# Kernel tuning notes

Hardware: AMD Instinct MI355X
Metric: run time of the kernel (lower is better)

Reference implementation:

```python
import jax, jax.numpy as jnp
import numpy as np

ANNEAL_T_START = 5.0
T_END = 1.0


def setup_inputs() -> dict:
    key = jax.random.key(0)
    ks = jax.random.split(key, 8)
    B, V, H, CD, WID = 8192, 1024, 128, 16, 64
    return {
        "cond": jax.random.normal(ks[0], (B, CD), jnp.float32),
        "W": 0.01 * jax.random.normal(ks[1], (V, H), jnp.float32),
        "b": 0.01 * jax.random.normal(ks[2], (V,), jnp.float32),
        "c": 0.01 * jax.random.normal(ks[3], (H,), jnp.float32),
        "fc1_w": jax.random.normal(ks[4], (WID, CD), jnp.float32) / np.float32(np.sqrt(CD)),
        "fc1_b": jnp.zeros((WID,), jnp.float32),
        "fc2_w": jax.random.normal(ks[5], (2 * (V + H), WID), jnp.float32) / np.float32(np.sqrt(WID)),
        "fc2_b": jnp.zeros((2 * (V + H),), jnp.float32),
        "falloff": jnp.float32(1.0),
        "steps": 16,
    }


def _bern(key, p):
    # Bernoulli sample as float of same dtype as p.
    return (jax.random.uniform(key, p.shape, p.dtype) < p).astype(p.dtype)


def reference(cond, W, b, c, fc1_w, fc1_b, fc2_w, fc2_b, falloff, steps):
    V, H = W.shape
    B = cond.shape[0]
    dtype = W.dtype

    # Conditioner: FiLM-style modulation of visible/hidden biases.
    x = jnp.tanh(cond @ fc1_w.T + fc1_b)
    x = x @ fc2_w.T + fc2_b  # [B, 2*(V+H)]
    gamma_b = x[:, :V]
    beta_b = x[:, V:2 * V]
    gamma_c = x[:, 2 * V:2 * V + H]
    beta_c = x[:, 2 * V + H:]
    b_mod = (1.0 + gamma_b) * b + beta_b  # [B, V]
    c_mod = (1.0 + gamma_c) * c + beta_c  # [B, H]
    bsum = jnp.sum(b_mod, axis=-1)  # [B], constant across steps

    # Annealing temperature schedule (sigmoid falloff).
    t = jnp.arange(steps, dtype=dtype)
    s = 1.0 / (1.0 + jnp.exp(falloff * (t - steps / 2.0)))
    temps = T_END + (ANNEAL_T_START - T_END) * s  # [steps]

    base = jax.random.key(42)
    v0 = _bern(jax.random.fold_in(base, 2 ** 20), jnp.full((B, V), 0.5, dtype))
    s0_0 = jnp.ones((B, 1), dtype)

    def flip(v, s0):
        return s0 * v + (1.0 - s0) * (1.0 - v)

    def step(carry, xs):
        v, s0 = carry
        i, T = xs
        k1, k2, k3 = jax.random.split(jax.random.fold_in(base, i), 3)
        v_eff = flip(v, s0)
        p_h = jax.nn.sigmoid((v_eff @ W + c_mod) / T)  # [B, H]
        h = _bern(k1, p_h)
        a = h @ W.T  # [B, V]
        vb = jnp.sum(v * b_mod, axis=-1)
        va = jnp.sum(v * a, axis=-1)
        dE = -bsum - jnp.sum(a, axis=-1) + 2.0 * vb + 2.0 * va  # [B]
        p_s0 = jax.nn.sigmoid(dE / T)
        s0n = _bern(k2, p_s0)[:, None]  # [B, 1]
        p_v = jax.nn.sigmoid((a + b_mod) / T)
        v_samp = _bern(k3, p_v)
        v_next = flip(v_samp, s0n)
        return (v_next, s0n), None

    (v, _), _ = jax.lax.scan(
        step, (v0, s0_0), (jnp.arange(steps, dtype=jnp.int32), temps)
    )
    return v
```

## Files before the change

### kernel.cpp

```cpp
#include <hip/hip_runtime.h>
#include <stdint.h>

#pragma clang fp contract(off)

#define B_ 8192
#define V_ 1024
#define H_ 128
#define CD_ 16
#define WID_ 64
#define NOUT_ 2304
#define STEPS_ 16

typedef float f32x2 __attribute__((ext_vector_type(2)));

__device__ __forceinline__ void pkfma(f32x2& acc, f32x2 wv, f32x2 bf2) {
  asm("v_pk_fma_f32 %0, %1, %2, %0" : "+v"(acc) : "v"(wv), "v"(bf2));
}

__host__ __device__ __forceinline__ void tf2x32(uint32_t k0, uint32_t k1,
                                                uint32_t x0, uint32_t x1,
                                                uint32_t* o0, uint32_t* o1) {
  uint32_t ks2 = k0 ^ k1 ^ 0x1BD11BDAu;
#define RL_(v, d) (((v) << (d)) | ((v) >> (32 - (d))))
#define RND_(a) { x0 += x1; x1 = RL_(x1, a); x1 ^= x0; }
  x0 += k0; x1 += k1;
  RND_(13) RND_(15) RND_(26) RND_(6)
  x0 += k1; x1 += ks2 + 1u;
  RND_(17) RND_(29) RND_(16) RND_(24)
  x0 += ks2; x1 += k0 + 2u;
  RND_(13) RND_(15) RND_(26) RND_(6)
  x0 += k0; x1 += k1 + 3u;
  RND_(17) RND_(29) RND_(16) RND_(24)
  x0 += k1; x1 += ks2 + 4u;
  RND_(13) RND_(15) RND_(26) RND_(6)
  x0 += ks2; x1 += k0 + 5u;
#undef RND_
#undef RL_
  *o0 = x0; *o1 = x1;
}

struct Keys { uint32_t a[6]; };

__device__ __forceinline__ uint32_t draw_bits(uint32_t ka, uint32_t kb, uint32_t j) {
  uint32_t x0, x1;
  tf2x32(ka, kb, 0u, j, &x0, &x1);
  return x0 ^ x1;
}

__device__ __forceinline__ float bits_to_u(uint32_t bits) {
  return __fsub_rn(__uint_as_float((bits >> 9) | 0x3f800000u), 1.0f);
}

__device__ __forceinline__ float exp_a(float x) {
  float xc = fminf(fmaxf(x, -88.3762626647949f), 88.3762626647950f);
  float fx = floorf(__fadd_rn(__fmul_rn(xc, 1.44269504088896341f), 0.5f));
  float xr = __fsub_rn(xc, __fmul_rn(0.693359375f, fx));
  xr = __fsub_rn(xr, __fmul_rn(-2.12194440e-4f, fx));
  float zz = __fmul_rn(xr, xr);
  float y = 1.9875691500E-4f;
  y = __fadd_rn(__fmul_rn(y, xr), 1.3981999507E-3f);
  y = __fadd_rn(__fmul_rn(y, xr), 8.3334519073E-3f);
  y = __fadd_rn(__fmul_rn(y, xr), 4.1665795894E-2f);
  y = __fadd_rn(__fmul_rn(y, xr), 1.6666665459E-1f);
  y = __fadd_rn(__fmul_rn(y, xr), 5.0000001201E-1f);
  y = __fadd_rn(__fmul_rn(y, zz), xr);
  y = __fadd_rn(y, 1.0f);
  int n = (int)fx;
  float sc = __int_as_float((n + 127) << 23);
  return __fmul_rn(y, sc);
}

__device__ __forceinline__ float tanh_a(float xin) {
  float x = fmaxf(fminf(xin, 7.90531110763549805f), -7.90531110763549805f);
  float x2 = __fmul_rn(x, x);
  float p = __fadd_rn(__fmul_rn(x2, -2.76076847742355e-16f), 2.00018790482477e-13f);
  p = __fadd_rn(__fmul_rn(x2, p), -8.60467152213735e-11f);
  p = __fadd_rn(__fmul_rn(x2, p), 5.12229709037114e-08f);
  p = __fadd_rn(__fmul_rn(x2, p), 1.48572235717979e-05f);
  p = __fadd_rn(__fmul_rn(x2, p), 6.37261928875436e-04f);
  p = __fadd_rn(__fmul_rn(x2, p), 4.89352455891786e-03f);
  p = __fmul_rn(x, p);
  float q = __fadd_rn(__fmul_rn(x2, 1.19825839466702e-06f), 1.18534705686654e-04f);
  q = __fadd_rn(__fmul_rn(x2, q), 2.26843463243900e-03f);
  q = __fadd_rn(__fmul_rn(x2, q), 4.89352518554385e-03f);
  float r = p / q;
  if (fabsf(xin) < 0.0004f) r = xin;
  return r;
}

__device__ __forceinline__ float sigmoid_a(float z) {
  float e = exp_a(-z);
  return 1.0f / __fadd_rn(1.0f, e);
}

__global__ void k_transpose(const float* __restrict__ W, float* __restrict__ WT,
                            const float* __restrict__ fc2w, float* __restrict__ fc2T) {
  int i = blockIdx.x * blockDim.x + threadIdx.x;
  if (i < V_ * H_) { int v = i / H_, h = i % H_; WT[h * V_ + v] = W[i]; }
  if (i < NOUT_ * WID_) { int j = i / WID_, w = i % WID_; fc2T[w * NOUT_ + j] = fc2w[i]; }
}

__global__ void k_temps(const float* __restrict__ falloff, float* __restrict__ temps) {
  int t = threadIdx.x;
  if (t < 16) {
    float arg = __fmul_rn(*falloff, __fsub_rn((float)t, 8.0f));
    float e = exp_a(arg);
    float s = 1.0f / __fadd_rn(1.0f, e);
    temps[t] = __fadd_rn(1.0f, __fmul_rn(4.0f, s));
  }
}

__global__ void k_mlp1(const float* __restrict__ cond, const float* __restrict__ fc1w,
                       const float* __restrict__ fc1b, float* __restrict__ xout) {
  int idx = blockIdx.x * blockDim.x + threadIdx.x;
  if (idx >= B_ * WID_) return;
  int row = idx >> 6, w = idx & 63;
  float acc = 0.0f;
  for (int k = 0; k < CD_; k++) acc = __fmaf_rn(cond[row * CD_ + k], fc1w[w * CD_ + k], acc);
  float z = __fadd_rn(acc, fc1b[w]);
  xout[idx] = tanh_a(z);
}

__global__ __launch_bounds__(128) void k_mlp2b(const float* __restrict__ xmlp,
                       const float* __restrict__ fc2T, const float* __restrict__ fc2b,
                       const float* __restrict__ bvec, float* __restrict__ b_mod) {
  __shared__ float xs[32][WID_];
  int jbase = blockIdx.x * 128;
  int r0 = blockIdx.y * 32;
  int tid = threadIdx.x;
  for (int t = tid; t < 32 * WID_; t += 128)
    xs[t >> 6][t & 63] = xmlp[(r0 + (t >> 6)) * WID_ + (t & 63)];
  __syncthreads();
  int j = jbase + tid;
  float accg[32], accb[32];
#pragma unroll
  for (int r = 0; r < 32; r++) { accg[r] = 0.0f; accb[r] = 0.0f; }
  for (int w = 0; w < WID_; w++) {
    float fg = fc2T[w * NOUT_ + j];
    float fb = fc2T[w * NOUT_ + 1024 + j];
#pragma unroll
    for (int r = 0; r < 32; r++) {
      float xv = xs[r][w];
      accg[r] = __fmaf_rn(xv, fg, accg[r]);
      accb[r] = __fmaf_rn(xv, fb, accb[r]);
    }
  }
  float bj = bvec[j];
  float biasg = fc2b[j], biasb = fc2b[1024 + j];
#pragma unroll
  for (int r = 0; r < 32; r++) {
    float g = __fadd_rn(accg[r], biasg);
    float bb = __fadd_rn(accb[r], biasb);
    float t1 = __fadd_rn(1.0f, g);
    b_mod[(r0 + r) * V_ + j] = __fadd_rn(__fmul_rn(t1, bj), bb);
  }
}

__global__ __launch_bounds__(128) void k_mlp2c(const float* __restrict__ xmlp,
                       const float* __restrict__ fc2T, const float* __restrict__ fc2b,
                       const float* __restrict__ cvec, float* __restrict__ c_mod) {
  __shared__ float xs[32][WID_];
  int r0 = blockIdx.y * 32;
  int tid = threadIdx.x;
  for (int t = tid; t < 32 * WID_; t += 128)
    xs[t >> 6][t & 63] = xmlp[(r0 + (t >> 6)) * WID_ + (t & 63)];
  __syncthreads();
  float accg[32], accb[32];
#pragma unroll
  for (int r = 0; r < 32; r++) { accg[r] = 0.0f; accb[r] = 0.0f; }
  for (int w = 0; w < WID_; w++) {
    float fg = fc2T[w * NOUT_ + 2048 + tid];
    float fb = fc2T[w * NOUT_ + 2176 + tid];
#pragma unroll
    for (int r = 0; r < 32; r++) {
      float xv = xs[r][w];
      accg[r] = __fmaf_rn(xv, fg, accg[r]);
      accb[r] = __fmaf_rn(xv, fb, accb[r]);
    }
  }
  float cj = cvec[tid];
  float biasg = fc2b[2048 + tid], biasb = fc2b[2176 + tid];
#pragma unroll
  for (int r = 0; r < 32; r++) {
    float g = __fadd_rn(accg[r], biasg);
    float bb = __fadd_rn(accb[r], biasb);
    float t1 = __fadd_rn(1.0f, g);
    c_mod[(r0 + r) * H_ + tid] = __fadd_rn(__fmul_rn(t1, cj), bb);
  }
}

__global__ __launch_bounds__(64) void k_bsum(const float* __restrict__ b_mod,
                                             float* __restrict__ bsum) {
  int row = blockIdx.x * 64 + threadIdx.x;
  const float4* bp = (const float4*)(b_mod + (size_t)row * V_);
  float acc = 0.0f;
  for (int c = 0; c < 32; c++) {
    float4 Bv[8];
#pragma unroll
    for (int q = 0; q < 8; q++) Bv[q] = bp[c * 8 + q];
#pragma unroll
    for (int q = 0; q < 8; q++) {
      acc = __fadd_rn(acc, Bv[q].x);
      acc = __fadd_rn(acc, Bv[q].y);
      acc = __fadd_rn(acc, Bv[q].z);
      acc = __fadd_rn(acc, Bv[q].w);
    }
  }
  bsum[row] = acc;
}

__global__ void k_v0(float* __restrict__ vout, uint32_t* __restrict__ v_bits,
                     float* __restrict__ s0, uint32_t kva, uint32_t kvb) {
  int idx = blockIdx.x * blockDim.x + threadIdx.x;
  int row = idx >> 10, col = idx & 1023;
  uint32_t bits = draw_bits(kva, kvb, (uint32_t)idx);
  float u = bits_to_u(bits);
  float v = (u < 0.5f) ? 1.0f : 0.0f;
  vout[idx] = v;
  unsigned long long m = __ballot(v == 1.0f);
  if ((threadIdx.x & 63) == 0) {
    v_bits[row * 32 + (col >> 5)] = (uint32_t)m;
    v_bits[row * 32 + (col >> 5) + 1] = (uint32_t)(m >> 32);
  }
  if (col == 0) s0[row] = 1.0f;
}

__global__ __launch_bounds__(128) void k_h(const float* __restrict__ W,
                   const float* __restrict__ c_mod, const uint32_t* __restrict__ v_bits,
                   const float* __restrict__ s0, uint32_t* __restrict__ h_bits,
                   const float* __restrict__ temps, int step, Keys kn) {
  __shared__ uint32_t nib[16][32];
  int tid = threadIdx.x;
  int ct = tid & 31;
  int rt = tid >> 5;
  int h0 = ct << 2;
  int row0 = blockIdx.x * 16 + rt * 4;
  float T = temps[step];
  f32x2 acc[4][2];
#pragma unroll
  for (int r = 0; r < 4; r++) { acc[r][0] = f32x2{0.f, 0.f}; acc[r][1] = f32x2{0.f, 0.f}; }
  uint32_t flip[4];
#pragma unroll
  for (int r = 0; r < 4; r++) flip[r] = (s0[row0 + r] == 0.0f) ? 0xFFFFFFFFu : 0u;
  const float* wbase = W + h0;

  auto sect = [&](uint32_t w0, uint32_t w1, uint32_t w2, uint32_t w3, const float* wp) {
    uint32_t m[4];
    m[0] = __brev(w0) ^ flip[0];
    m[1] = __brev(w1) ^ flip[1];
    m[2] = __brev(w2) ^ flip[2];
    m[3] = __brev(w3) ^ flip[3];
    for (int j4 = 0; j4 < 8; j4++) {
#pragma unroll
      for (int jj = 0; jj < 4; jj++) {
        float4 wv = *(const float4*)(wp + (size_t)jj * H_);
        f32x2 wlo = {wv.x, wv.y};
        f32x2 whi = {wv.z, wv.w};
#pragma unroll
        for (int r = 0; r < 4; r++) {
          uint32_t sm = (uint32_t)((int32_t)m[r] >> 31);
          m[r] <<= 1;
          float bf = __uint_as_float(sm & 0x3f800000u);
          f32x2 b2 = {bf, bf};
          pkfma(acc[r][0], wlo, b2);
          pkfma(acc[r][1], whi, b2);
        }
      }
      wp += (size_t)4 * H_;
    }
  };

  const uint4* vb0 = (const uint4*)(v_bits + (size_t)row0 * 32);
  const uint4* vb1 = (const uint4*)(v_bits + (size_t)(row0 + 1) * 32);
  const uint4* vb2 = (const uint4*)(v_bits + (size_t)(row0 + 2) * 32);
  const uint4* vb3 = (const uint4*)(v_bits + (size_t)(row0 + 3) * 32);
  for (int kq = 0; kq < 8; kq++) {
    uint4 q0 = vb0[kq];
    uint4 q1 = vb1[kq];
    uint4 q2 = vb2[kq];
    uint4 q3 = vb3[kq];
    const float* wk = wbase + (size_t)(kq * 128) * H_;
    sect(q0.x, q1.x, q2.x, q3.x, wk);
    sect(q0.y, q1.y, q2.y, q3.y, wk + (size_t)32 * H_);
    sect(q0.z, q1.z, q2.z, q3.z, wk + (size_t)64 * H_);
    sect(q0.w, q1.w, q2.w, q3.w, wk + (size_t)96 * H_);
  }

#pragma unroll
  for (int r = 0; r < 4; r++) {
    int row = row0 + r;
    float4 cm = *(const float4*)(c_mod + (size_t)row * H_ + h0);
    const float cma[4] = {cm.x, cm.y, cm.z, cm.w};
    const float ac[4] = {acc[r][0][0], acc[r][0][1], acc[r][1][0], acc[r][1][1]};
    uint32_t nb = 0;
#pragma unroll
    for (int e = 0; e < 4; e++) {
      float z = __fadd_rn(ac[e], cma[e]) / T;
      float p = sigmoid_a(z);
      uint32_t b = draw_bits(kn.a[0], kn.a[1], (uint32_t)(row * H_ + h0 + e));
      if (bits_to_u(b) < p) nb |= 1u << e;
    }
    nib[rt * 4 + r][ct] = nb;
  }
  __syncthreads();
  if (tid < 64) {
    int rloc = tid >> 2, wq = tid & 3;
    uint32_t word = 0;
#pragma unroll
    for (int i = 0; i < 8; i++) word |= nib[rloc][wq * 8 + i] << (4 * i);
    h_bits[(size_t)(blockIdx.x * 16 + rloc) * 4 + wq] = word;
  }
}

__global__ __launch_bounds__(256) void k_a(const float* __restrict__ WT,
                   const uint32_t* __restrict__ h_bits, float* __restrict__ a) {
  int tid = threadIdx.x;
  int ct = tid & 63;
  int rt = tid >> 6;
  int v0 = blockIdx.x * 256 + (ct << 2);
  int r0 = blockIdx.y * 32 + rt * 8;
  f32x2 acc[8][2];
#pragma unroll
  for (int r = 0; r < 8; r++) { acc[r][0] = f32x2{0.f, 0.f}; acc[r][1] = f32x2{0.f, 0.f}; }
  uint4 hw[8];
#pragma unroll
  for (int r = 0; r < 8; r++) hw[r] = *(const uint4*)(h_bits + (size_t)(r0 + r) * 4);
  const float* wp0 = WT + v0;

  auto asect = [&](int WW, const uint32_t mwin[8]) {
    uint32_t m[8];
#pragma unroll
    for (int r = 0; r < 8; r++) m[r] = __brev(mwin[r]);
    const float* wp = wp0 + (size_t)(WW * 32) * V_;
    for (int j4 = 0; j4 < 8; j4++) {
#pragma unroll
      for (int jj = 0; jj < 4; jj++) {
        float4 wv = *(const float4*)(wp + (size_t)jj * V_);
        f32x2 wlo = {wv.x, wv.y};
        f32x2 whi = {wv.z, wv.w};
#pragma unroll
        for (int r = 0; r < 8; r++) {
          uint32_t sm = (uint32_t)((int32_t)m[r] >> 31);
          m[r] <<= 1;
          float bf = __uint_as_float(sm & 0x3f800000u);
          f32x2 b2 = {bf, bf};
          pkfma(acc[r][0], wlo, b2);
          pkfma(acc[r][1], whi, b2);
        }
      }
      wp += (size_t)4 * V_;
    }
  };

  {
    uint32_t mw[8];
#pragma unroll
    for (int r = 0; r < 8; r++) mw[r] = hw[r].x;
    asect(0, mw);
#pragma unroll
    for (int r = 0; r < 8; r++) mw[r] = hw[r].y;
    asect(1, mw);
#pragma unroll
    for (int r = 0; r < 8; r++) mw[r] = hw[r].z;
    asect(2, mw);
#pragma unroll
    for (int r = 0; r < 8; r++) mw[r] = hw[r].w;
    asect(3, mw);
  }

#pragma unroll
  for (int r = 0; r < 8; r++) {
    float4 o = make_float4(acc[r][0][0], acc[r][0][1], acc[r][1][0], acc[r][1][1]);
    *(float4*)(a + (size_t)(r0 + r) * V_ + v0) = o;
  }
}

__global__ __launch_bounds__(64) void k_s0(const float* __restrict__ a,
                     const float* __restrict__ b_mod, const float* __restrict__ bsum,
                     const uint32_t* __restrict__ v_bits, float* __restrict__ s0,
                     const float* __restrict__ temps, int step, Keys kn) {
  int row = blockIdx.x * 64 + threadIdx.x;
  const float4* ap = (const float4*)(a + (size_t)row * V_);
  const float4* bp = (const float4*)(b_mod + (size_t)row * V_);
  const uint32_t* vbp = v_bits + row * 32;
  float suma = 0.0f, vb = 0.0f, va = 0.0f;
  float4 A0[8], B0[8], A1[8], B1[8];
  uint32_t m0, m1;

  auto LOADC = [&](int c, float4* A, float4* B, uint32_t& m) {
#pragma unroll
    for (int q = 0; q < 8; q++) { A[q] = ap[c * 8 + q]; B[q] = bp[c * 8 + q]; }
    m = vbp[c];
  };
  auto PROC = [&](const float4* A, const float4* B, uint32_t m) {
#pragma unroll
    for (int q = 0; q < 8; q++) {
      const float ax[4] = {A[q].x, A[q].y, A[q].z, A[q].w};
      const float bx[4] = {B[q].x, B[q].y, B[q].z, B[q].w};
#pragma unroll
      for (int e = 0; e < 4; e++) {
        float bit = (float)((m >> (q * 4 + e)) & 1u);
        suma = __fadd_rn(suma, ax[e]);
        vb = __fmaf_rn(bx[e], bit, vb);
        va = __fmaf_rn(ax[e], bit, va);
      }
    }
  };

  LOADC(0, A0, B0, m0);
  for (int cc = 0; cc < 16; cc++) {
    LOADC(2 * cc + 1, A1, B1, m1);
    PROC(A0, B0, m0);
    if (cc < 15) LOADC(2 * cc + 2, A0, B0, m0);
    PROC(A1, B1, m1);
  }

  float dE = __fsub_rn(-bsum[row], suma);
  dE = __fadd_rn(dE, __fmul_rn(2.0f, vb));
  dE = __fadd_rn(dE, __fmul_rn(2.0f, va));
  float T = temps[step];
  float p = sigmoid_a(dE / T);
  uint32_t bits = draw_bits(kn.a[2], kn.a[3], (uint32_t)row);
  float u = bits_to_u(bits);
  s0[row] = (u < p) ? 1.0f : 0.0f;
}

__global__ void k_v(const float* __restrict__ a, const float* __restrict__ b_mod,
                    const float* __restrict__ s0, float* __restrict__ vout,
                    uint32_t* __restrict__ v_bits, const float* __restrict__ temps, int step,
                    Keys kn) {
  int idx = blockIdx.x * blockDim.x + threadIdx.x;
  int row = idx >> 10, col = idx & 1023;
  float T = temps[step];
  float z = __fadd_rn(a[idx], b_mod[idx]) / T;
  float p = sigmoid_a(z);
  uint32_t bits = draw_bits(kn.a[4], kn.a[5], (uint32_t)idx);
  float u = bits_to_u(bits);
  float vs = (u < p) ? 1.0f : 0.0f;
  float vn = (s0[row] != 0.0f) ? vs : (1.0f - vs);
  vout[idx] = vn;
  unsigned long long m = __ballot(vn == 1.0f);
  if ((threadIdx.x & 63) == 0) {
    v_bits[row * 32 + (col >> 5)] = (uint32_t)m;
    v_bits[row * 32 + (col >> 5) + 1] = (uint32_t)(m >> 32);
  }
}

extern "C" void kernel_launch(void* const* d_in, const int* in_sizes, int n_in,
                              void* d_out, int out_size, void* d_ws, size_t ws_size,
                              hipStream_t stream) {
  const float* cond = (const float*)d_in[0];
  const float* W = (const float*)d_in[1];
  const float* bvec = (const float*)d_in[2];
  const float* cvec = (const float*)d_in[3];
  const float* fc1w = (const float*)d_in[4];
  const float* fc1b = (const float*)d_in[5];
  const float* fc2w = (const float*)d_in[6];
  const float* fc2b = (const float*)d_in[7];
  const float* falloff = (const float*)d_in[8];
  float* out = (float*)d_out;

  char* ws = (char*)d_ws;
  size_t off = 0;
  auto alloc = [&](size_t bytes) { void* p = ws + off; off += (bytes + 255) & ~(size_t)255; return p; };
  float* b_mod = (float*)alloc((size_t)B_ * V_ * 4);
  float* c_mod = (float*)alloc((size_t)B_ * H_ * 4);
  float* abuf  = (float*)alloc((size_t)B_ * V_ * 4);
  float* xmlp  = (float*)alloc((size_t)B_ * WID_ * 4);
  float* bsum  = (float*)alloc((size_t)B_ * 4);
  float* s0    = (float*)alloc((size_t)B_ * 4);
  uint32_t* v_bits = (uint32_t*)alloc((size_t)B_ * 32 * 4);
  uint32_t* h_bits = (uint32_t*)alloc((size_t)B_ * 4 * 4);
  float* WT    = (float*)alloc((size_t)H_ * V_ * 4);
  float* fc2T  = (float*)alloc((size_t)WID_ * NOUT_ * 4);
  float* temps = (float*)alloc(16 * 4);

  uint32_t kva, kvb;
  tf2x32(0u, 42u, 0u, 1048576u, &kva, &kvb);
  Keys kn[16];
  for (int i = 0; i < 16; i++) {
    uint32_t f0, f1;
    tf2x32(0u, 42u, 0u, (uint32_t)i, &f0, &f1);
    uint32_t a0, a1;
    tf2x32(f0, f1, 0u, 0u, &a0, &a1); kn[i].a[0] = a0; kn[i].a[1] = a1;
    tf2x32(f0, f1, 0u, 1u, &a0, &a1); kn[i].a[2] = a0; kn[i].a[3] = a1;
    tf2x32(f0, f1, 0u, 2u, &a0, &a1); kn[i].a[4] = a0; kn[i].a[5] = a1;
  }

  k_transpose<<<(NOUT_ * WID_ + 255) / 256, 256, 0, stream>>>(W, WT, fc2w, fc2T);
  k_temps<<<1, 64, 0, stream>>>(falloff, temps);
  k_mlp1<<<(B_ * WID_) / 256, 256, 0, stream>>>(cond, fc1w, fc1b, xmlp);
  k_mlp2b<<<dim3(8, 256), 128, 0, stream>>>(xmlp, fc2T, fc2b, bvec, b_mod);
  k_mlp2c<<<dim3(1, 256), 128, 0, stream>>>(xmlp, fc2T, fc2b, cvec, c_mod);
  k_bsum<<<B_ / 64, 64, 0, stream>>>(b_mod, bsum);
  k_v0<<<(B_ * V_) / 256, 256, 0, stream>>>(out, v_bits, s0, kva, kvb);

  for (int i = 0; i < STEPS_; i++) {
    k_h<<<B_ / 16, 128, 0, stream>>>(W, c_mod, v_bits, s0, h_bits, temps, i, kn[i]);
    k_a<<<dim3(4, B_ / 32), 256, 0, stream>>>(WT, h_bits, abuf);
    k_s0<<<B_ / 64, 64, 0, stream>>>(abuf, b_mod, bsum, v_bits, s0, temps, i, kn[i]);
    k_v<<<(B_ * V_) / 256, 256, 0, stream>>>(abuf, b_mod, s0, out, v_bits, temps, i, kn[i]);
  }
}
```

Baseline: 3.580 ms.

## Stage W tiles in double-buffered shared memory for hidden-unit kernel

The hidden-activation kernel now loads W in 64-row tiles into a double-buffered LDS array, prefetching the next tile into registers while computing on the current one. The block size doubles to 256 threads covering 32 batch rows, so each W tile is reused across more rows. The aim is to cut repeated global/L2 reads of W per block. The trade-offs are 64KB of LDS per block, which limits occupancy, and an extra barrier per tile.

```diff
diff --git a/kernel.cpp b/kernel.cpp
--- a/kernel.cpp
+++ b/kernel.cpp
@@ -225,16 +225,16 @@
   if (col == 0) s0[row] = 1.0f;
 }
 
-__global__ __launch_bounds__(128) void k_h(const float* __restrict__ W,
+__global__ __launch_bounds__(256) void k_h(const float* __restrict__ W,
                    const float* __restrict__ c_mod, const uint32_t* __restrict__ v_bits,
                    const float* __restrict__ s0, uint32_t* __restrict__ h_bits,
                    const float* __restrict__ temps, int step, Keys kn) {
-  __shared__ uint32_t nib[16][32];
+  __shared__ float Wt[2][64 * H_];
   int tid = threadIdx.x;
   int ct = tid & 31;
   int rt = tid >> 5;
   int h0 = ct << 2;
-  int row0 = blockIdx.x * 16 + rt * 4;
+  int row0 = blockIdx.x * 32 + rt * 4;
   float T = temps[step];
   f32x2 acc[4][2];
 #pragma unroll
@@ -242,18 +242,32 @@
   uint32_t flip[4];
 #pragma unroll
   for (int r = 0; r < 4; r++) flip[r] = (s0[row0 + r] == 0.0f) ? 0xFFFFFFFFu : 0u;
-  const float* wbase = W + h0;
-
-  auto sect = [&](uint32_t w0, uint32_t w1, uint32_t w2, uint32_t w3, const float* wp) {
-    uint32_t m[4];
-    m[0] = __brev(w0) ^ flip[0];
-    m[1] = __brev(w1) ^ flip[1];
-    m[2] = __brev(w2) ^ flip[2];
-    m[3] = __brev(w3) ^ flip[3];
-    for (int j4 = 0; j4 < 8; j4++) {
-#pragma unroll
-      for (int jj = 0; jj < 4; jj++) {
-        float4 wv = *(const float4*)(wp + (size_t)jj * H_);
+
+  float4 st[8];
+  auto stage_load = [&](int tile) {
+    const float4* src = (const float4*)(W + (size_t)tile * 64 * H_);
+#pragma unroll
+    for (int i = 0; i < 8; i++) st[i] = src[tid + i * 256];
+  };
+  auto stage_store = [&](int bsel) {
+    float4* dst = (float4*)&Wt[bsel][0];
+#pragma unroll
+    for (int i = 0; i < 8; i++) dst[tid + i * 256] = st[i];
+  };
+  auto compute_tile = [&](int bsel, int tile) {
+    uint2 mwr[4];
+#pragma unroll
+    for (int r = 0; r < 4; r++)
+      mwr[r] = *(const uint2*)(v_bits + (size_t)(row0 + r) * 32 + tile * 2);
+#pragma unroll
+    for (int w2 = 0; w2 < 2; w2++) {
+      uint32_t m[4];
+#pragma unroll
+      for (int r = 0; r < 4; r++)
+        m[r] = __brev(w2 ? mwr[r].y : mwr[r].x) ^ flip[r];
+#pragma unroll 8
+      for (int j = 0; j < 32; j++) {
+        float4 wv = *(const float4*)(&Wt[bsel][(w2 * 32 + j) * H_ + h0]);
         f32x2 wlo = {wv.x, wv.y};
         f32x2 whi = {wv.z, wv.w};
 #pragma unroll
@@ -266,26 +280,20 @@
           pkfma(acc[r][1], whi, b2);
         }
       }
-      wp += (size_t)4 * H_;
     }
   };
 
-  const uint4* vb0 = (const uint4*)(v_bits + (size_t)row0 * 32);
-  const uint4* vb1 = (const uint4*)(v_bits + (size_t)(row0 + 1) * 32);
-  const uint4* vb2 = (const uint4*)(v_bits + (size_t)(row0 + 2) * 32);
-  const uint4* vb3 = (const uint4*)(v_bits + (size_t)(row0 + 3) * 32);
-  for (int kq = 0; kq < 8; kq++) {
-    uint4 q0 = vb0[kq];
-    uint4 q1 = vb1[kq];
-    uint4 q2 = vb2[kq];
-    uint4 q3 = vb3[kq];
-    const float* wk = wbase + (size_t)(kq * 128) * H_;
-    sect(q0.x, q1.x, q2.x, q3.x, wk);
-    sect(q0.y, q1.y, q2.y, q3.y, wk + (size_t)32 * H_);
-    sect(q0.z, q1.z, q2.z, q3.z, wk + (size_t)64 * H_);
-    sect(q0.w, q1.w, q2.w, q3.w, wk + (size_t)96 * H_);
-  }
-
+  stage_load(0);
+  stage_store(0);
+  __syncthreads();
+  for (int t = 0; t < 16; t++) {
+    if (t < 15) stage_load(t + 1);
+    compute_tile(t & 1, t);
+    if (t < 15) stage_store((t + 1) & 1);
+    __syncthreads();
+  }
+
+  uint32_t* nib = (uint32_t*)&Wt[0][0];
 #pragma unroll
   for (int r = 0; r < 4; r++) {
     int row = row0 + r;
@@ -300,15 +308,15 @@
       uint32_t b = draw_bits(kn.a[0], kn.a[1], (uint32_t)(row * H_ + h0 + e));
       if (bits_to_u(b) < p) nb |= 1u << e;
     }
-    nib[rt * 4 + r][ct] = nb;
+    nib[(rt * 4 + r) * 32 + ct] = nb;
   }
   __syncthreads();
-  if (tid < 64) {
+  if (tid < 128) {
     int rloc = tid >> 2, wq = tid & 3;
     uint32_t word = 0;
 #pragma unroll
-    for (int i = 0; i < 8; i++) word |= nib[rloc][wq * 8 + i] << (4 * i);
-    h_bits[(size_t)(blockIdx.x * 16 + rloc) * 4 + wq] = word;
+    for (int i = 0; i < 8; i++) word |= nib[rloc * 32 + wq * 8 + i] << (4 * i);
+    h_bits[(size_t)(blockIdx.x * 32 + rloc) * 4 + wq] = word;
   }
 }
 
@@ -496,7 +504,7 @@
   k_v0<<<(B_ * V_) / 256, 256, 0, stream>>>(out, v_bits, s0, kva, kvb);
 
   for (int i = 0; i < STEPS_; i++) {
-    k_h<<<B_ / 16, 128, 0, stream>>>(W, c_mod, v_bits, s0, h_bits, temps, i, kn[i]);
+    k_h<<<B_ / 32, 256, 0, stream>>>(W, c_mod, v_bits, s0, h_bits, temps, i, kn[i]);
     k_a<<<dim3(4, B_ / 32), 256, 0, stream>>>(WT, h_bits, abuf);
     k_s0<<<B_ / 64, 64, 0, stream>>>(abuf, b_mod, bsum, v_bits, s0, temps, i, kn[i]);
     k_v<<<(B_ * V_) / 256, 256, 0, stream>>>(abuf, b_mod, s0, out, v_bits, temps, i, kn[i]);
```

New measurement: 3.449 ms. 3.6% less time.
